# Kernel optimization log

Hardware: AMD Instinct MI355X
Metric: run time of the kernel (lower is better)

Reference implementation:

```python
import jax, jax.numpy as jnp
import numpy as np

N_NODES = 32768
N_EDGES = 524288
IN_CH = 128
OUT_CH = 128
EDGE_CH = 64
HIDDEN = 128


def setup_inputs() -> dict:
    key = jax.random.key(0)
    ks = jax.random.split(key, 8)
    x = jax.random.normal(ks[0], (N_NODES, IN_CH), dtype=jnp.float32)
    edge_index = jax.random.randint(ks[1], (2, N_EDGES), 0, N_NODES, dtype=jnp.int64)
    edge_attr = jax.random.uniform(ks[2], (N_EDGES, EDGE_CH), dtype=jnp.float32)
    # filter_network: Linear(edge_ch, hidden) -> tanh -> Linear(hidden, out)
    s1 = 1.0 / np.sqrt(EDGE_CH)
    s2 = 1.0 / np.sqrt(HIDDEN)
    W1 = jax.random.uniform(ks[3], (EDGE_CH, HIDDEN), jnp.float32, -s1, s1)
    b1 = jax.random.uniform(ks[4], (HIDDEN,), jnp.float32, -s1, s1)
    W2 = jax.random.uniform(ks[5], (HIDDEN, OUT_CH), jnp.float32, -s2, s2)
    b2 = jax.random.uniform(ks[6], (OUT_CH,), jnp.float32, -s2, s2)
    # attention_vector [out, 1], xavier_uniform with gain 1.414
    lim = 1.414 * np.sqrt(6.0 / (OUT_CH + 1))
    attn = jax.random.uniform(ks[7], (OUT_CH,), jnp.float32, -lim, lim)
    return {"x": x, "edge_index": edge_index, "edge_attr": edge_attr,
            "W1": W1, "b1": b1, "W2": W2, "b2": b2, "attn": attn}


def _segment_softmax(scores, segment_ids, num_segments):
    # PyG-style numerically stable softmax over segments
    seg_max = jax.ops.segment_max(scores, segment_ids, num_segments=num_segments)
    seg_max = jnp.where(jnp.isfinite(seg_max), seg_max, 0.0)
    e = jnp.exp(scores - seg_max[segment_ids])
    denom = jax.ops.segment_sum(e, segment_ids, num_segments=num_segments)
    return e / (denom[segment_ids] + 1e-16)


def reference(x, edge_index, edge_attr, W1, b1, W2, b2, attn):
    source, target = edge_index[0], edge_index[1]
    n_nodes = x.shape[0]
    source_features = x[source]                                  # [E, in]
    edge_attr_norm = edge_attr / (jnp.linalg.norm(edge_attr, axis=-1, keepdims=True) + 1e-8)
    h = jnp.tanh(edge_attr_norm @ W1 + b1)                       # [E, hidden]
    edge_filters = h @ W2 + b2                                   # [E, out]
    messages = source_features * edge_filters                    # [E, out]
    attention_scores = messages @ attn                           # [E]
    attention_weights = _segment_softmax(attention_scores, target, n_nodes)
    messages = messages * attention_weights[:, None]
    output = jax.ops.segment_sum(messages, target, num_segments=n_nodes)  # [N, out]
    return output, attention_weights
```

## Files before the change

kernel.cpp:

```cpp
#include <hip/hip_runtime.h>
#include <stdint.h>

typedef short short8 __attribute__((ext_vector_type(8)));
typedef float f32x16 __attribute__((ext_vector_type(16)));
typedef unsigned ux4 __attribute__((ext_vector_type(4)));

__device__ __forceinline__ unsigned cvtpk(float lo, float hi){
  unsigned r;
  asm("v_cvt_pk_bf16_f32 %0, %1, %2" : "=v"(r) : "v"(lo), "v"(hi));
  return r;
}

__device__ __forceinline__ short8 frag_from(unsigned a, unsigned b, unsigned c, unsigned d){
  union { unsigned u[4]; short8 s; } t;
  t.u[0] = a; t.u[1] = b; t.u[2] = c; t.u[3] = d;
  return t.s;
}

__global__ void k_setup(const float* __restrict__ x, uint2* __restrict__ xb, int n4,
                        const int* __restrict__ ei, int* __restrict__ rowptr, int E,
                        const float* __restrict__ W1, const float* __restrict__ W2,
                        ux4* __restrict__ Wf)
{
  const long long tid = (long long)blockIdx.x * 256 + threadIdx.x;
  if (tid < 48 * 64) {
    const int f = (int)(tid >> 6), l = (int)(tid & 63);
    const int r = l & 31, hh = l >> 5;
    float v[8];
    if (f < 16) {
      const int mf = f >> 2, ks = f & 3;
      const int c = 32 * mf + r, kb = ks * 16 + hh * 8;
#pragma unroll
      for (int j = 0; j < 8; ++j) v[j] = W1[(kb + j) * 128 + c];
    } else {
      const int f2 = f - 16, mf2 = f2 >> 3, ks = f2 & 7;
      const int o = 32 * mf2 + r, cb = ks * 16 + hh * 8;
#pragma unroll
      for (int j = 0; j < 8; ++j) v[j] = W2[(cb + j) * 128 + o];
    }
    ux4 d;
    d.x = cvtpk(v[0], v[1]); d.y = cvtpk(v[2], v[3]);
    d.z = cvtpk(v[4], v[5]); d.w = cvtpk(v[6], v[7]);
    Wf[(long long)f * 64 + l] = d;
  }
  const long long tot = (n4 > E) ? n4 : E;
  for (long long i = tid; i < tot; i += (long long)gridDim.x * 256) {
    if (i < n4) {
      float4 v = ((const float4*)x)[i];
      uint2 o; o.x = cvtpk(v.x, v.y); o.y = cvtpk(v.z, v.w);
      xb[i] = o;
    }
    if (i < E) atomicAdd(&rowptr[ei[E + i]], 1);
  }
}

__global__ __launch_bounds__(1024)
void k_scan(int* __restrict__ p, int N){
  __shared__ int ls[1024];
  const int t = threadIdx.x;
  const int chunk = (N + 1023) >> 10;
  const int c0 = t * chunk, c1 = min(N, c0 + chunk);
  int s = 0;
  for (int i = c0; i < c1; ++i) s += p[i];
  ls[t] = s;
  __syncthreads();
  for (int off = 1; off < 1024; off <<= 1) {
    int add = (t >= off) ? ls[t - off] : 0;
    __syncthreads();
    ls[t] += add;
    __syncthreads();
  }
  int run = (t == 0) ? 0 : ls[t - 1];
  for (int i = c0; i < c1; ++i) { int v = p[i]; p[i] = run; run += v; }
}

__global__ void k_fill(const int* __restrict__ ei, int* __restrict__ rowptr,
                       int* __restrict__ pose, int* __restrict__ eidx, int E){
  for (long long i = (long long)blockIdx.x * 256 + threadIdx.x; i < E;
       i += (long long)gridDim.x * 256) {
    int tg = ei[E + i];
    int pos = atomicAdd(&rowptr[tg], 1);
    if (pose) pose[i] = pos;
    eidx[pos] = (int)i;
  }
}

#define K1B 512
__global__ __launch_bounds__(K1B)
void k1_fused(const unsigned* __restrict__ xb, const int* __restrict__ ei,
              const float* __restrict__ ea, const ux4* __restrict__ Wf,
              const float* __restrict__ b1, const float* __restrict__ b2,
              const float* __restrict__ attn, const int* __restrict__ eidx,
              unsigned* __restrict__ msgp, float* __restrict__ scoreS, int E)
{
  __shared__ ux4 sWf[48 * 64];
  for (int i = threadIdx.x; i < 48 * 64; i += K1B) sWf[i] = Wf[i];
  __syncthreads();

  const int lane = threadIdx.x & 63;
  const int wv   = threadIdx.x >> 6;
  const int h    = lane >> 5;
  const int r31  = lane & 31;
  const long long gstep = (long long)gridDim.x * (K1B / 64) * 32;
  long long p = ((long long)blockIdx.x * (K1B / 64) + wv) * 32 + r31;
  if (p - r31 >= E) return;

  int eC = eidx[(p < E) ? p : (long long)(E - 1)];
  int srcC = ei[eC];
  unsigned ebC[4][4]; float rinC;
  {
    const float* er = ea + (long long)eC * 64 + h * 8;
    float4 v[8];
#pragma unroll
    for (int ks = 0; ks < 4; ++ks) {
      v[2*ks]   = *(const float4*)(er + ks * 16);
      v[2*ks+1] = *(const float4*)(er + ks * 16 + 4);
    }
    float ss = 0.f;
#pragma unroll
    for (int k8 = 0; k8 < 8; ++k8) {
      ss = fmaf(v[k8].x, v[k8].x, ss); ss = fmaf(v[k8].y, v[k8].y, ss);
      ss = fmaf(v[k8].z, v[k8].z, ss); ss = fmaf(v[k8].w, v[k8].w, ss);
    }
    ss += __shfl_xor(ss, 32);
    rinC = 1.0f / (sqrtf(ss) + 1e-8f);
#pragma unroll
    for (int ks = 0; ks < 4; ++ks) {
      ebC[ks][0] = cvtpk(v[2*ks].x,   v[2*ks].y);
      ebC[ks][1] = cvtpk(v[2*ks].z,   v[2*ks].w);
      ebC[ks][2] = cvtpk(v[2*ks+1].x, v[2*ks+1].y);
      ebC[ks][3] = cvtpk(v[2*ks+1].z, v[2*ks+1].w);
    }
  }
  long long pn = p + gstep;
  bool hasN = (pn - r31) < E;
  int eN = 0;
  if (hasN) eN = eidx[(pn < E) ? pn : (long long)(E - 1)];

  while (true) {
    float4 eaN[8]; int srcN = 0;
    if (hasN) {
      srcN = ei[eN];
      const float* er = ea + (long long)eN * 64 + h * 8;
#pragma unroll
      for (int ks = 0; ks < 4; ++ks) {
        eaN[2*ks]   = *(const float4*)(er + ks * 16);
        eaN[2*ks+1] = *(const float4*)(er + ks * 16 + 4);
      }
    }
    long long pnn = pn + gstep;
    bool hasNN = hasN && ((pnn - r31) < E);
    int eNN = 0;
    if (hasNN) eNN = eidx[(pnn < E) ? pnn : (long long)(E - 1)];

    const unsigned* xrow = xb + (long long)srcC * 64;
    uint2 xw[4];
#pragma unroll
    for (int rq = 0; rq < 4; ++rq)
      xw[rq] = *(const uint2*)(xrow + (8*rq + 4*h) / 2);
    asm volatile("" ::: "memory");

    unsigned hb[8][4];
#pragma unroll
    for (int mf = 0; mf < 4; ++mf) {
      f32x16 a1;
#pragma unroll
      for (int i = 0; i < 16; ++i) a1[i] = 0.f;
#pragma unroll
      for (int ks = 0; ks < 4; ++ks) {
        ux4 w = sWf[(mf * 4 + ks) * 64 + lane];
        a1 = __builtin_amdgcn_mfma_f32_32x32x16_bf16(
            frag_from(w.x, w.y, w.z, w.w),
            frag_from(ebC[ks][0], ebC[ks][1], ebC[ks][2], ebC[ks][3]), a1, 0, 0, 0);
      }
      float hv[16];
#pragma unroll
      for (int rq = 0; rq < 4; ++rq) {
        float4 bc = *(const float4*)(b1 + 32*mf + 8*rq + 4*h);
#pragma unroll
        for (int i = 0; i < 4; ++i) {
          float pre = fmaf(a1[rq*4+i], rinC, ((const float*)&bc)[i]);
          float e2  = __expf(2.0f * pre);
          hv[rq*4+i] = 1.0f - 2.0f / (e2 + 1.0f);
        }
      }
#pragma unroll
      for (int q = 0; q < 2; ++q) {
        unsigned A = cvtpk(hv[q*8+0], hv[q*8+1]);
        unsigned B = cvtpk(hv[q*8+2], hv[q*8+3]);
        unsigned C = cvtpk(hv[q*8+4], hv[q*8+5]);
        unsigned D = cvtpk(hv[q*8+6], hv[q*8+7]);
        unsigned Axr = (unsigned)__shfl_xor((int)A, 32);
        unsigned Bxr = (unsigned)__shfl_xor((int)B, 32);
        unsigned Cxr = (unsigned)__shfl_xor((int)C, 32);
        unsigned Dxr = (unsigned)__shfl_xor((int)D, 32);
        hb[2*mf+q][0] = h ? Cxr : A;
        hb[2*mf+q][1] = h ? Dxr : B;
        hb[2*mf+q][2] = h ? C   : Axr;
        hb[2*mf+q][3] = h ? D   : Bxr;
      }
    }

    float score = 0.f;
#pragma unroll
    for (int mf2 = 0; mf2 < 4; ++mf2) {
      uint2 xwN[4];
      if (mf2 < 3) {
#pragma unroll
        for (int rq = 0; rq < 4; ++rq)
          xwN[rq] = *(const uint2*)(xrow + (32*(mf2+1) + 8*rq + 4*h) / 2);
      }
      f32x16 a2;
#pragma unroll
      for (int i = 0; i < 16; ++i) a2[i] = 0.f;
#pragma unroll
      for (int ks = 0; ks < 8; ++ks) {
        ux4 w = sWf[(16 + mf2 * 8 + ks) * 64 + lane];
        a2 = __builtin_amdgcn_mfma_f32_32x32x16_bf16(
            frag_from(w.x, w.y, w.z, w.w),
            frag_from(hb[ks][0], hb[ks][1], hb[ks][2], hb[ks][3]), a2, 0, 0, 0);
      }
      unsigned pk[8];
#pragma unroll
      for (int rq = 0; rq < 4; ++rq) {
        const int o0 = 32*mf2 + 8*rq + 4*h;
        float4 b2c = *(const float4*)(b2 + o0);
        float4 atc = *(const float4*)(attn + o0);
        float x0 = __uint_as_float(xw[rq].x << 16);
        float x1 = __uint_as_float(xw[rq].x & 0xffff0000u);
        float x2 = __uint_as_float(xw[rq].y << 16);
        float x3 = __uint_as_float(xw[rq].y & 0xffff0000u);
        float m0 = (a2[rq*4+0] + b2c.x) * x0;
        float m1 = (a2[rq*4+1] + b2c.y) * x1;
        float m2 = (a2[rq*4+2] + b2c.z) * x2;
        float m3 = (a2[rq*4+3] + b2c.w) * x3;
        score = fmaf(m0, atc.x, score);
        score = fmaf(m1, atc.y, score);
        score = fmaf(m2, atc.z, score);
        score = fmaf(m3, atc.w, score);
        pk[2*rq]   = cvtpk(m0, m1);
        pk[2*rq+1] = cvtpk(m2, m3);
      }
      if (p < E) {
        ux4* dst = (ux4*)(msgp + p * 64 + 16*mf2 + 8*h);
        ux4 s0, s1;
        s0.x = pk[0]; s0.y = pk[1]; s0.z = pk[2]; s0.w = pk[3];
        s1.x = pk[4]; s1.y = pk[5]; s1.z = pk[6]; s1.w = pk[7];
        dst[0] = s0; dst[1] = s1;
      }
      if (mf2 < 3) {
#pragma unroll
        for (int rq = 0; rq < 4; ++rq) xw[rq] = xwN[rq];
      }
    }
    score += __shfl_xor(score, 32);
    if (h == 0 && p < E) scoreS[p] = score;

    if (!hasN) break;
    float ss = 0.f;
#pragma unroll
    for (int k8 = 0; k8 < 8; ++k8) {
      ss = fmaf(eaN[k8].x, eaN[k8].x, ss); ss = fmaf(eaN[k8].y, eaN[k8].y, ss);
      ss = fmaf(eaN[k8].z, eaN[k8].z, ss); ss = fmaf(eaN[k8].w, eaN[k8].w, ss);
    }
    ss += __shfl_xor(ss, 32);
    rinC = 1.0f / (sqrtf(ss) + 1e-8f);
#pragma unroll
    for (int ks = 0; ks < 4; ++ks) {
      ebC[ks][0] = cvtpk(eaN[2*ks].x,   eaN[2*ks].y);
      ebC[ks][1] = cvtpk(eaN[2*ks].z,   eaN[2*ks].w);
      ebC[ks][2] = cvtpk(eaN[2*ks+1].x, eaN[2*ks+1].y);
      ebC[ks][3] = cvtpk(eaN[2*ks+1].z, eaN[2*ks+1].w);
    }
    srcC = srcN; p = pn; pn = pnn; hasN = hasNN; eN = eNN;
  }
}

template<int FUSEW>
__global__ __launch_bounds__(256)
void k_gather(const unsigned* __restrict__ msgp, const float* __restrict__ scoreS,
              const int* __restrict__ rowptr, const int* __restrict__ eidx,
              float* __restrict__ lse, float* __restrict__ wreg,
              float* __restrict__ out, int N)
{
  const int lane = threadIdx.x & 63;
  const int node = blockIdx.x * 4 + (threadIdx.x >> 6);
  if (node >= N) return;
  const int end   = rowptr[node];
  const int start = node ? rowptr[node - 1] : 0;
  const int L     = end - start;

  float2 acc; acc.x = 0.f; acc.y = 0.f;

  if (L <= 64) {
    float sc = (lane < L) ? scoreS[start + lane] : -3.4e38f;
    float mn = sc;
#pragma unroll
    for (int off = 32; off; off >>= 1) mn = fmaxf(mn, __shfl_xor(mn, off));
    float ex = (lane < L) ? __expf(sc - mn) : 0.f;
    float s = ex;
#pragma unroll
    for (int off = 32; off; off >>= 1) s += __shfl_xor(s, off);
    const float w = ex / (s + 1e-16f);
    if (FUSEW) {
      if (lane < L) wreg[eidx[start + lane]] = w;
    } else if (lane == 0) {
      lse[node] = mn + logf(s + 1e-16f);
    }
#pragma unroll 4
    for (int j2 = 0; j2 < L; ++j2) {
      float wj = __shfl(w, j2);
      unsigned md = msgp[(long long)(start + j2) * 64 + lane];
      acc.x = fmaf(wj, __uint_as_float(md << 16),          acc.x);
      acc.y = fmaf(wj, __uint_as_float(md & 0xffff0000u), acc.y);
    }
  } else {
    float m = -3.4e38f, s = 0.f;
    for (int c0 = 0; c0 < L; c0 += 64) {
      const int j = c0 + lane;
      float sc = (j < L) ? scoreS[start + j] : -3.4e38f;
      float cm = sc;
#pragma unroll
      for (int off = 32; off; off >>= 1) cm = fmaxf(cm, __shfl_xor(cm, off));
      const float mn = fmaxf(m, cm);
      float ex = (j < L) ? __expf(sc - mn) : 0.f;
#pragma unroll
      for (int off = 32; off; off >>= 1) ex += __shfl_xor(ex, off);
      s = s * __expf(m - mn) + ex;
      m = mn;
    }
    const float lsev = m + logf(s + 1e-16f);
    if (!FUSEW && lane == 0) lse[node] = lsev;

    for (int c0 = 0; c0 < L; c0 += 64) {
      const int j = c0 + lane;
      float w = (j < L) ? __expf(scoreS[start + j] - lsev) : 0.f;
      if (FUSEW && j < L) wreg[eidx[start + j]] = w;
      const int jn = min(64, L - c0);
#pragma unroll 4
      for (int j2 = 0; j2 < jn; ++j2) {
        float wj = __shfl(w, j2);
        unsigned md = msgp[(long long)(start + c0 + j2) * 64 + lane];
        acc.x = fmaf(wj, __uint_as_float(md << 16),          acc.x);
        acc.y = fmaf(wj, __uint_as_float(md & 0xffff0000u), acc.y);
      }
    }
  }
  const int mf2 = lane >> 4, hh = (lane >> 3) & 1, rq = (lane >> 1) & 3, half = lane & 1;
  const int ch0 = 32*mf2 + 8*rq + 4*hh + 2*half;
  *(float2*)(out + (long long)node * 128 + ch0) = acc;
}

__global__ void k_wfin(int* __restrict__ pw, const int* __restrict__ ei,
                       const float* __restrict__ scoreS, const float* __restrict__ lse,
                       int E){
  for (long long i = (long long)blockIdx.x * 256 + threadIdx.x; i < E;
       i += (long long)gridDim.x * 256) {
    int pos = pw[i];
    float w = __expf(scoreS[pos] - lse[ei[E + i]]);
    pw[i] = __float_as_int(w);
  }
}

extern "C" void kernel_launch(void* const* d_in, const int* in_sizes, int n_in,
                              void* d_out, int out_size, void* d_ws, size_t ws_size,
                              hipStream_t stream)
{
  const float* x    = (const float*)d_in[0];
  const int*   ei   = (const int*)d_in[1];
  const float* ea   = (const float*)d_in[2];
  const float* W1   = (const float*)d_in[3];
  const float* b1   = (const float*)d_in[4];
  const float* W2   = (const float*)d_in[5];
  const float* b2   = (const float*)d_in[6];
  const float* attn = (const float*)d_in[7];
  const int N = in_sizes[0] / 128;
  const int E = in_sizes[2] / 64;
  if (E <= 0 || N <= 0) return;

  float* out   = (float*)d_out;
  float* wregN = out + (long long)N * 128;
  ux4*     Wf     = (ux4*)d_out;
  size_t   offE   = 65536;
  int*     eidxDO = (int*)((char*)d_out + offE);
  size_t   offX   = (offE + (size_t)E * 4 + 255) & ~(size_t)255;
  unsigned* xb    = (unsigned*)((char*)d_out + offX);

  char* wsb = (char*)d_ws;
  unsigned* msgp   = (unsigned*)wsb;
  float*    scoreS = (float*)(wsb + (size_t)E * 256);
  int*      rowptr = (int*)(wsb + (size_t)E * 260);
  float*    lse    = (float*)(wsb + (size_t)E * 260 + (size_t)N * 4);
  int*      eidxWS = (int*)(wsb + (size_t)E * 260 + (size_t)N * 8);
  const size_t need1 = (size_t)E * 260 + (size_t)N * 8;
  const size_t need2 = need1 + (size_t)E * 4;
  if (ws_size < need1) return;
  if ((size_t)out_size < (size_t)N * 128 + (size_t)E) return;
  if ((size_t)N * 512 < offX + (size_t)N * 256) return;

  const bool fused = (ws_size >= need2);
  int* eidx = fused ? eidxWS : eidxDO;

  (void)hipMemsetAsync(rowptr, 0, (size_t)N * 4, stream);
  k_setup<<<1024, 256, 0, stream>>>(x, (uint2*)xb, N * 32, ei, rowptr, E, W1, W2, Wf);
  k_scan<<<1, 1024, 0, stream>>>(rowptr, N);
  k_fill<<<1024, 256, 0, stream>>>(ei, rowptr, fused ? nullptr : (int*)wregN, eidx, E);
  const long long nwaves = ((long long)E + 31) / 32;
  const int grid = (int)min((long long)512, (nwaves + (K1B/64) - 1) / (K1B/64));
  k1_fused<<<grid, K1B, 0, stream>>>(xb, ei, ea, Wf, b1, b2, attn,
                                     eidx, msgp, scoreS, E);
  if (fused) {
    k_gather<1><<<(N + 3) / 4, 256, 0, stream>>>(msgp, scoreS, rowptr, eidx,
                                                 lse, wregN, out, N);
  } else {
    k_gather<0><<<(N + 3) / 4, 256, 0, stream>>>(msgp, scoreS, rowptr, eidx,
                                                 lse, wregN, out, N);
    k_wfin<<<1024, 256, 0, stream>>>((int*)wregN, ei, scoreS, lse, E);
  }
}
```

Baseline: 267.6 us.

## Fuse edge MLP and per-node softmax aggregation into one tiled LDS kernel

Replaces the separate edge-MLP kernel and gather kernel with one kernel. Each block takes windows of CSR-sorted edges (about WIN edges snapped to node boundaries), computes messages into LDS in a swizzled layout, then does the segment softmax and weighted sum directly from LDS. This removes the global round trip of the bf16 message buffer (E×256 bytes) and one launch. Nodes with more than CAP edges fall back to a chunked online-softmax path across the whole block. In exchange it loses the software prefetch pipelining of the old MLP loop, uses 1024-thread blocks with large LDS and a grid of at most 256 blocks, and tile boundaries come from atomicMin in the scan.

```diff
diff --git a/kernel.cpp b/kernel.cpp
--- a/kernel.cpp
+++ b/kernel.cpp
@@ -4,6 +4,19 @@
 typedef short short8 __attribute__((ext_vector_type(8)));
 typedef float f32x16 __attribute__((ext_vector_type(16)));
 typedef unsigned ux4 __attribute__((ext_vector_type(4)));
+
+#define WIN  288
+#define CAP  384
+#define FBLK 1024
+
+#define OFF_WF    0
+#define OFF_MSG   49152
+#define OFF_SC    (OFF_MSG + CAP*64*4)
+#define OFF_RED   (OFF_SC + CAP*4)
+#define OFF_CTL   (OFF_RED + 64)
+#define OFF_PART  (OFF_CTL + 16)
+#define OFF_ACC   (OFF_PART + 16*128*4)
+#define LDS_TOT   (OFF_ACC + 512)
 
 __device__ __forceinline__ unsigned cvtpk(float lo, float hi){
   unsigned r;
@@ -55,7 +68,7 @@
 }
 
 __global__ __launch_bounds__(1024)
-void k_scan(int* __restrict__ p, int N){
+void k_scan(int* __restrict__ p, int N, int* __restrict__ tileFirst, int ntiles){
   __shared__ int ls[1024];
   const int t = threadIdx.x;
   const int chunk = (N + 1023) >> 10;
@@ -71,294 +84,339 @@
     __syncthreads();
   }
   int run = (t == 0) ? 0 : ls[t - 1];
-  for (int i = c0; i < c1; ++i) { int v = p[i]; p[i] = run; run += v; }
+  for (int i = c0; i < c1; ++i) {
+    int v = p[i];
+    p[i] = run;
+    int tw = run / WIN;
+    if (tw > ntiles - 1) tw = ntiles - 1;
+    atomicMin(&tileFirst[tw], i);
+    run += v;
+  }
 }
 
 __global__ void k_fill(const int* __restrict__ ei, int* __restrict__ rowptr,
-                       int* __restrict__ pose, int* __restrict__ eidx, int E){
+                       int* __restrict__ eidx, int E){
   for (long long i = (long long)blockIdx.x * 256 + threadIdx.x; i < E;
        i += (long long)gridDim.x * 256) {
     int tg = ei[E + i];
     int pos = atomicAdd(&rowptr[tg], 1);
-    if (pose) pose[i] = pos;
     eidx[pos] = (int)i;
   }
 }
 
-#define K1B 512
-__global__ __launch_bounds__(K1B)
-void k1_fused(const unsigned* __restrict__ xb, const int* __restrict__ ei,
-              const float* __restrict__ ea, const ux4* __restrict__ Wf,
-              const float* __restrict__ b1, const float* __restrict__ b2,
-              const float* __restrict__ attn, const int* __restrict__ eidx,
-              unsigned* __restrict__ msgp, float* __restrict__ scoreS, int E)
+__device__ __forceinline__ void mlp_chunk(
+    int e0, int cnt, int oversized,
+    const unsigned* __restrict__ xb, const int* __restrict__ ei,
+    const float* __restrict__ ea, const float* __restrict__ b1,
+    const float* __restrict__ b2, const float* __restrict__ attn,
+    const int* __restrict__ eidx, float* __restrict__ scoreS,
+    const ux4* sWf, unsigned* sMsg, float* sScore,
+    int lane, int wv, int h, int r31)
 {
-  __shared__ ux4 sWf[48 * 64];
-  for (int i = threadIdx.x; i < 48 * 64; i += K1B) sWf[i] = Wf[i];
-  __syncthreads();
-
-  const int lane = threadIdx.x & 63;
-  const int wv   = threadIdx.x >> 6;
+  if (wv * 32 >= cnt) return;
+  const int li  = wv * 32 + r31;
+  const int lic = (li < cnt) ? li : (cnt - 1);
+  const long long p = (long long)e0 + lic;
+  const int e   = eidx[p];
+  const int src = ei[e];
+
+  const float* er = ea + (long long)e * 64 + h * 8;
+  float4 v[8];
+#pragma unroll
+  for (int ks = 0; ks < 4; ++ks) {
+    v[2*ks]   = *(const float4*)(er + ks * 16);
+    v[2*ks+1] = *(const float4*)(er + ks * 16 + 4);
+  }
+  float ss = 0.f;
+#pragma unroll
+  for (int k8 = 0; k8 < 8; ++k8) {
+    ss = fmaf(v[k8].x, v[k8].x, ss); ss = fmaf(v[k8].y, v[k8].y, ss);
+    ss = fmaf(v[k8].z, v[k8].z, ss); ss = fmaf(v[k8].w, v[k8].w, ss);
+  }
+  ss += __shfl_xor(ss, 32);
+  const float rin = 1.0f / (sqrtf(ss) + 1e-8f);
+  unsigned eb[4][4];
+#pragma unroll
+  for (int ks = 0; ks < 4; ++ks) {
+    eb[ks][0] = cvtpk(v[2*ks].x,   v[2*ks].y);
+    eb[ks][1] = cvtpk(v[2*ks].z,   v[2*ks].w);
+    eb[ks][2] = cvtpk(v[2*ks+1].x, v[2*ks+1].y);
+    eb[ks][3] = cvtpk(v[2*ks+1].z, v[2*ks+1].w);
+  }
+
+  unsigned hb[8][4];
+#pragma unroll
+  for (int mf = 0; mf < 4; ++mf) {
+    f32x16 a1;
+#pragma unroll
+    for (int i = 0; i < 16; ++i) a1[i] = 0.f;
+#pragma unroll
+    for (int ks = 0; ks < 4; ++ks) {
+      ux4 w = sWf[(mf * 4 + ks) * 64 + lane];
+      a1 = __builtin_amdgcn_mfma_f32_32x32x16_bf16(
+          frag_from(w.x, w.y, w.z, w.w),
+          frag_from(eb[ks][0], eb[ks][1], eb[ks][2], eb[ks][3]), a1, 0, 0, 0);
+    }
+    float hv[16];
+#pragma unroll
+    for (int rq = 0; rq < 4; ++rq) {
+      float4 bc = *(const float4*)(b1 + 32*mf + 8*rq + 4*h);
+#pragma unroll
+      for (int i = 0; i < 4; ++i) {
+        float pre = fmaf(a1[rq*4+i], rin, ((const float*)&bc)[i]);
+        float e2  = __expf(2.0f * pre);
+        hv[rq*4+i] = 1.0f - 2.0f / (e2 + 1.0f);
+      }
+    }
+#pragma unroll
+    for (int q = 0; q < 2; ++q) {
+      unsigned A = cvtpk(hv[q*8+0], hv[q*8+1]);
+      unsigned B = cvtpk(hv[q*8+2], hv[q*8+3]);
+      unsigned C = cvtpk(hv[q*8+4], hv[q*8+5]);
+      unsigned D = cvtpk(hv[q*8+6], hv[q*8+7]);
+      unsigned Axr = (unsigned)__shfl_xor((int)A, 32);
+      unsigned Bxr = (unsigned)__shfl_xor((int)B, 32);
+      unsigned Cxr = (unsigned)__shfl_xor((int)C, 32);
+      unsigned Dxr = (unsigned)__shfl_xor((int)D, 32);
+      hb[2*mf+q][0] = h ? Cxr : A;
+      hb[2*mf+q][1] = h ? Dxr : B;
+      hb[2*mf+q][2] = h ? C   : Axr;
+      hb[2*mf+q][3] = h ? D   : Bxr;
+    }
+  }
+
+  const unsigned* xrow = xb + (long long)src * 64;
+  float score = 0.f;
+#pragma unroll
+  for (int mf2 = 0; mf2 < 4; ++mf2) {
+    uint2 xw[4];
+#pragma unroll
+    for (int rq = 0; rq < 4; ++rq)
+      xw[rq] = *(const uint2*)(xrow + (32*mf2 + 8*rq + 4*h) / 2);
+    f32x16 a2;
+#pragma unroll
+    for (int i = 0; i < 16; ++i) a2[i] = 0.f;
+#pragma unroll
+    for (int ks = 0; ks < 8; ++ks) {
+      ux4 w = sWf[(16 + mf2 * 8 + ks) * 64 + lane];
+      a2 = __builtin_amdgcn_mfma_f32_32x32x16_bf16(
+          frag_from(w.x, w.y, w.z, w.w),
+          frag_from(hb[ks][0], hb[ks][1], hb[ks][2], hb[ks][3]), a2, 0, 0, 0);
+    }
+    unsigned pk[8];
+#pragma unroll
+    for (int rq = 0; rq < 4; ++rq) {
+      const int o0 = 32*mf2 + 8*rq + 4*h;
+      float4 b2c = *(const float4*)(b2 + o0);
+      float4 atc = *(const float4*)(attn + o0);
+      float x0 = __uint_as_float(xw[rq].x << 16);
+      float x1 = __uint_as_float(xw[rq].x & 0xffff0000u);
+      float x2 = __uint_as_float(xw[rq].y << 16);
+      float x3 = __uint_as_float(xw[rq].y & 0xffff0000u);
+      float m0 = (a2[rq*4+0] + b2c.x) * x0;
+      float m1 = (a2[rq*4+1] + b2c.y) * x1;
+      float m2 = (a2[rq*4+2] + b2c.z) * x2;
+      float m3 = (a2[rq*4+3] + b2c.w) * x3;
+      score = fmaf(m0, atc.x, score);
+      score = fmaf(m1, atc.y, score);
+      score = fmaf(m2, atc.z, score);
+      score = fmaf(m3, atc.w, score);
+      pk[2*rq]   = cvtpk(m0, m1);
+      pk[2*rq+1] = cvtpk(m2, m3);
+    }
+    const int s0slot = 4*mf2 + 2*h;
+    const int m15 = li & 15;
+    ux4 q0, q1;
+    q0.x = pk[0]; q0.y = pk[1]; q0.z = pk[2]; q0.w = pk[3];
+    q1.x = pk[4]; q1.y = pk[5]; q1.z = pk[6]; q1.w = pk[7];
+    *(ux4*)&sMsg[li*64 + ((s0slot     ^ m15) << 2)] = q0;
+    *(ux4*)&sMsg[li*64 + (((s0slot+1) ^ m15) << 2)] = q1;
+  }
+  score += __shfl_xor(score, 32);
+  if (h == 0) {
+    sScore[li] = score;
+    if (oversized && li < cnt) scoreS[p] = score;
+  }
+}
+
+__device__ __forceinline__ unsigned msg_ld(const unsigned* sMsg, int row, int lane){
+  return sMsg[row*64 + ((((lane>>2) ^ (row & 15)) << 2) | (lane & 3))];
+}
+
+__global__ __launch_bounds__(FBLK)
+void k_fused(const unsigned* __restrict__ xb, const int* __restrict__ ei,
+             const float* __restrict__ ea, const ux4* __restrict__ Wf,
+             const float* __restrict__ b1, const float* __restrict__ b2,
+             const float* __restrict__ attn, const int* __restrict__ eidx,
+             const int* __restrict__ rowptr, const int* __restrict__ tileFirst,
+             float* __restrict__ scoreS, float* __restrict__ wreg,
+             float* __restrict__ out, int N, int E, int ntiles)
+{
+  extern __shared__ char smem[];
+  ux4*      sWf    = (ux4*)(smem + OFF_WF);
+  unsigned* sMsg   = (unsigned*)(smem + OFF_MSG);
+  float*    sScore = (float*)(smem + OFF_SC);
+  float*    sRed   = (float*)(smem + OFF_RED);
+  float*    sCtl   = (float*)(smem + OFF_CTL);
+  float*    sPart  = (float*)(smem + OFF_PART);
+  float*    sAcc   = (float*)(smem + OFF_ACC);
+
+  const int tid  = threadIdx.x;
+  const int lane = tid & 63;
+  const int wv   = tid >> 6;
   const int h    = lane >> 5;
   const int r31  = lane & 31;
-  const long long gstep = (long long)gridDim.x * (K1B / 64) * 32;
-  long long p = ((long long)blockIdx.x * (K1B / 64) + wv) * 32 + r31;
-  if (p - r31 >= E) return;
-
-  int eC = eidx[(p < E) ? p : (long long)(E - 1)];
-  int srcC = ei[eC];
-  unsigned ebC[4][4]; float rinC;
-  {
-    const float* er = ea + (long long)eC * 64 + h * 8;
-    float4 v[8];
-#pragma unroll
-    for (int ks = 0; ks < 4; ++ks) {
-      v[2*ks]   = *(const float4*)(er + ks * 16);
-      v[2*ks+1] = *(const float4*)(er + ks * 16 + 4);
-    }
-    float ss = 0.f;
-#pragma unroll
-    for (int k8 = 0; k8 < 8; ++k8) {
-      ss = fmaf(v[k8].x, v[k8].x, ss); ss = fmaf(v[k8].y, v[k8].y, ss);
-      ss = fmaf(v[k8].z, v[k8].z, ss); ss = fmaf(v[k8].w, v[k8].w, ss);
-    }
-    ss += __shfl_xor(ss, 32);
-    rinC = 1.0f / (sqrtf(ss) + 1e-8f);
-#pragma unroll
-    for (int ks = 0; ks < 4; ++ks) {
-      ebC[ks][0] = cvtpk(v[2*ks].x,   v[2*ks].y);
-      ebC[ks][1] = cvtpk(v[2*ks].z,   v[2*ks].w);
-      ebC[ks][2] = cvtpk(v[2*ks+1].x, v[2*ks+1].y);
-      ebC[ks][3] = cvtpk(v[2*ks+1].z, v[2*ks+1].w);
-    }
-  }
-  long long pn = p + gstep;
-  bool hasN = (pn - r31) < E;
-  int eN = 0;
-  if (hasN) eN = eidx[(pn < E) ? pn : (long long)(E - 1)];
-
-  while (true) {
-    float4 eaN[8]; int srcN = 0;
-    if (hasN) {
-      srcN = ei[eN];
-      const float* er = ea + (long long)eN * 64 + h * 8;
-#pragma unroll
-      for (int ks = 0; ks < 4; ++ks) {
-        eaN[2*ks]   = *(const float4*)(er + ks * 16);
-        eaN[2*ks+1] = *(const float4*)(er + ks * 16 + 4);
+
+  for (int i = tid; i < 48*64; i += FBLK) sWf[i] = Wf[i];
+  __syncthreads();
+
+  for (int t = blockIdx.x; t < ntiles; t += gridDim.x) {
+    const int nF = tileFirst[t];
+    if (nF >= N) continue;
+    int t2 = t + 1;
+    while (t2 < ntiles && tileFirst[t2] >= N) ++t2;
+    const int nL = (t2 < ntiles) ? tileFirst[t2] - 1 : N - 1;
+
+    int n  = nF;
+    int s0 = n ? rowptr[n-1] : 0;
+    while (n <= nL) {
+      const int en = rowptr[n];
+      const int dn = en - s0;
+      if (dn > CAP) {
+        if (tid < 128) sAcc[tid] = 0.f;
+        if (tid == 0) { sCtl[0] = -3.4e38f; sCtl[1] = 0.f; }
+        __syncthreads();
+        for (int c0 = 0; c0 < dn; c0 += CAP) {
+          const int cnt = min(CAP, dn - c0);
+          mlp_chunk(s0 + c0, cnt, 1, xb, ei, ea, b1, b2, attn, eidx, scoreS,
+                    sWf, sMsg, sScore, lane, wv, h, r31);
+          __syncthreads();
+          float vmax = (tid < cnt) ? sScore[tid] : -3.4e38f;
+#pragma unroll
+          for (int off = 32; off; off >>= 1) vmax = fmaxf(vmax, __shfl_xor(vmax, off));
+          if (lane == 0) sRed[wv] = vmax;
+          __syncthreads();
+          if (tid == 0) {
+            float cm = sRed[0];
+            for (int w = 1; w < 16; ++w) cm = fmaxf(cm, sRed[w]);
+            float mn = fmaxf(sCtl[0], cm);
+            sCtl[2] = __expf(sCtl[0] - mn);
+            sCtl[0] = mn;
+          }
+          __syncthreads();
+          const float mn = sCtl[0], r = sCtl[2];
+          float ev = (tid < cnt) ? __expf(sScore[tid] - mn) : 0.f;
+#pragma unroll
+          for (int off = 32; off; off >>= 1) ev += __shfl_xor(ev, off);
+          if (lane == 0) sRed[wv] = ev;
+          float2 pacc; pacc.x = 0.f; pacc.y = 0.f;
+          if (wv * 32 < cnt) {
+            float pl = (lane < 32 && wv*32 + lane < cnt)
+                     ? __expf(sScore[wv*32 + lane] - mn) : 0.f;
+            const int jn = min(32, cnt - wv*32);
+            for (int j2 = 0; j2 < jn; ++j2) {
+              float pj = __shfl(pl, j2);
+              unsigned md = msg_ld(sMsg, wv*32 + j2, lane);
+              pacc.x = fmaf(pj, __uint_as_float(md << 16),          pacc.x);
+              pacc.y = fmaf(pj, __uint_as_float(md & 0xffff0000u), pacc.y);
+            }
+          }
+          sPart[wv*128 + 2*lane]     = pacc.x;
+          sPart[wv*128 + 2*lane + 1] = pacc.y;
+          __syncthreads();
+          if (tid == 0) {
+            float ssum = 0.f;
+            for (int w = 0; w < 16; ++w) ssum += sRed[w];
+            sCtl[1] = sCtl[1] * sCtl[2] + ssum;
+          }
+          if (tid < 128) {
+            float tp = 0.f;
+            for (int w = 0; w < 16; ++w) tp += sPart[w*128 + tid];
+            sAcc[tid] = sAcc[tid] * r + tp;
+          }
+          __syncthreads();
+        }
+        const float mfin = sCtl[0];
+        const float sfin = sCtl[1] + 1e-16f;
+        for (int j = tid; j < dn; j += FBLK)
+          wreg[eidx[s0 + j]] = __expf(scoreS[s0 + j] - mfin) / sfin;
+        if (tid < 64) {
+          const int mf2 = tid >> 4, hh = (tid >> 3) & 1, rq = (tid >> 1) & 3, hf = tid & 1;
+          const int ch0 = 32*mf2 + 8*rq + 4*hh + 2*hf;
+          float2 o; o.x = sAcc[2*tid]; o.y = sAcc[2*tid + 1];
+          *(float2*)(out + (long long)n * 128 + ch0) = o;
+        }
+        __syncthreads();
+        s0 = en; ++n;
+        continue;
       }
-    }
-    long long pnn = pn + gstep;
-    bool hasNN = hasN && ((pnn - r31) < E);
-    int eNN = 0;
-    if (hasNN) eNN = eidx[(pnn < E) ? pnn : (long long)(E - 1)];
-
-    const unsigned* xrow = xb + (long long)srcC * 64;
-    uint2 xw[4];
-#pragma unroll
-    for (int rq = 0; rq < 4; ++rq)
-      xw[rq] = *(const uint2*)(xrow + (8*rq + 4*h) / 2);
-    asm volatile("" ::: "memory");
-
-    unsigned hb[8][4];
-#pragma unroll
-    for (int mf = 0; mf < 4; ++mf) {
-      f32x16 a1;
-#pragma unroll
-      for (int i = 0; i < 16; ++i) a1[i] = 0.f;
-#pragma unroll
-      for (int ks = 0; ks < 4; ++ks) {
-        ux4 w = sWf[(mf * 4 + ks) * 64 + lane];
-        a1 = __builtin_amdgcn_mfma_f32_32x32x16_bf16(
-            frag_from(w.x, w.y, w.z, w.w),
-            frag_from(ebC[ks][0], ebC[ks][1], ebC[ks][2], ebC[ks][3]), a1, 0, 0, 0);
+      int m = n, send = en;
+      while (m < nL) {
+        int nx = rowptr[m + 1];
+        if (nx - s0 > CAP) break;
+        send = nx; ++m;
       }
-      float hv[16];
-#pragma unroll
-      for (int rq = 0; rq < 4; ++rq) {
-        float4 bc = *(const float4*)(b1 + 32*mf + 8*rq + 4*h);
-#pragma unroll
-        for (int i = 0; i < 4; ++i) {
-          float pre = fmaf(a1[rq*4+i], rinC, ((const float*)&bc)[i]);
-          float e2  = __expf(2.0f * pre);
-          hv[rq*4+i] = 1.0f - 2.0f / (e2 + 1.0f);
+      mlp_chunk(s0, send - s0, 0, xb, ei, ea, b1, b2, attn, eidx, scoreS,
+                sWf, sMsg, sScore, lane, wv, h, r31);
+      __syncthreads();
+      for (int nn = n + wv; nn <= m; nn += 16) {
+        const int gs = nn ? rowptr[nn - 1] : 0;
+        const int L  = rowptr[nn] - gs;
+        const int ls = gs - s0;
+        float2 acc; acc.x = 0.f; acc.y = 0.f;
+        if (L <= 64) {
+          float sc = (lane < L) ? sScore[ls + lane] : -3.4e38f;
+          float mn = sc;
+#pragma unroll
+          for (int off = 32; off; off >>= 1) mn = fmaxf(mn, __shfl_xor(mn, off));
+          float ex = (lane < L) ? __expf(sc - mn) : 0.f;
+          float s = ex;
+#pragma unroll
+          for (int off = 32; off; off >>= 1) s += __shfl_xor(s, off);
+          const float w = ex / (s + 1e-16f);
+          if (lane < L) wreg[eidx[gs + lane]] = w;
+          for (int j2 = 0; j2 < L; ++j2) {
+            float wj = __shfl(w, j2);
+            unsigned md = msg_ld(sMsg, ls + j2, lane);
+            acc.x = fmaf(wj, __uint_as_float(md << 16),          acc.x);
+            acc.y = fmaf(wj, __uint_as_float(md & 0xffff0000u), acc.y);
+          }
+        } else {
+          float mr = -3.4e38f, s = 0.f;
+          for (int c0 = 0; c0 < L; c0 += 64) {
+            const int j = c0 + lane;
+            float sc = (j < L) ? sScore[ls + j] : -3.4e38f;
+            float cm = sc;
+#pragma unroll
+            for (int off = 32; off; off >>= 1) cm = fmaxf(cm, __shfl_xor(cm, off));
+            const float mn = fmaxf(mr, cm);
+            float ex = (j < L) ? __expf(sc - mn) : 0.f;
+#pragma unroll
+            for (int off = 32; off; off >>= 1) ex += __shfl_xor(ex, off);
+            s = s * __expf(mr - mn) + ex;
+            mr = mn;
+          }
+          const float inv = 1.0f / (s + 1e-16f);
+          for (int c0 = 0; c0 < L; c0 += 64) {
+            const int j = c0 + lane;
+            float w = (j < L) ? __expf(sScore[ls + j] - mr) * inv : 0.f;
+            if (j < L) wreg[eidx[gs + j]] = w;
+            const int jn = min(64, L - c0);
+            for (int j2 = 0; j2 < jn; ++j2) {
+              float wj = __shfl(w, j2);
+              unsigned md = msg_ld(sMsg, ls + c0 + j2, lane);
+              acc.x = fmaf(wj, __uint_as_float(md << 16),          acc.x);
+              acc.y = fmaf(wj, __uint_as_float(md & 0xffff0000u), acc.y);
+            }
+          }
         }
+        const int mf2 = lane >> 4, hh = (lane >> 3) & 1, rq = (lane >> 1) & 3, hf = lane & 1;
+        const int ch0 = 32*mf2 + 8*rq + 4*hh + 2*hf;
+        *(float2*)(out + (long long)nn * 128 + ch0) = acc;
       }
-#pragma unroll
-      for (int q = 0; q < 2; ++q) {
-        unsigned A = cvtpk(hv[q*8+0], hv[q*8+1]);
-        unsigned B = cvtpk(hv[q*8+2], hv[q*8+3]);
-        unsigned C = cvtpk(hv[q*8+4], hv[q*8+5]);
-        unsigned D = cvtpk(hv[q*8+6], hv[q*8+7]);
-        unsigned Axr = (unsigned)__shfl_xor((int)A, 32);
-        unsigned Bxr = (unsigned)__shfl_xor((int)B, 32);
-        unsigned Cxr = (unsigned)__shfl_xor((int)C, 32);
-        unsigned Dxr = (unsigned)__shfl_xor((int)D, 32);
-        hb[2*mf+q][0] = h ? Cxr : A;
-        hb[2*mf+q][1] = h ? Dxr : B;
-        hb[2*mf+q][2] = h ? C   : Axr;
-        hb[2*mf+q][3] = h ? D   : Bxr;
-      }
-    }
-
-    float score = 0.f;
-#pragma unroll
-    for (int mf2 = 0; mf2 < 4; ++mf2) {
-      uint2 xwN[4];
-      if (mf2 < 3) {
-#pragma unroll
-        for (int rq = 0; rq < 4; ++rq)
-          xwN[rq] = *(const uint2*)(xrow + (32*(mf2+1) + 8*rq + 4*h) / 2);
-      }
-      f32x16 a2;
-#pragma unroll
-      for (int i = 0; i < 16; ++i) a2[i] = 0.f;
-#pragma unroll
-      for (int ks = 0; ks < 8; ++ks) {
-        ux4 w = sWf[(16 + mf2 * 8 + ks) * 64 + lane];
-        a2 = __builtin_amdgcn_mfma_f32_32x32x16_bf16(
-            frag_from(w.x, w.y, w.z, w.w),
-            frag_from(hb[ks][0], hb[ks][1], hb[ks][2], hb[ks][3]), a2, 0, 0, 0);
-      }
-      unsigned pk[8];
-#pragma unroll
-      for (int rq = 0; rq < 4; ++rq) {
-        const int o0 = 32*mf2 + 8*rq + 4*h;
-        float4 b2c = *(const float4*)(b2 + o0);
-        float4 atc = *(const float4*)(attn + o0);
-        float x0 = __uint_as_float(xw[rq].x << 16);
-        float x1 = __uint_as_float(xw[rq].x & 0xffff0000u);
-        float x2 = __uint_as_float(xw[rq].y << 16);
-        float x3 = __uint_as_float(xw[rq].y & 0xffff0000u);
-        float m0 = (a2[rq*4+0] + b2c.x) * x0;
-        float m1 = (a2[rq*4+1] + b2c.y) * x1;
-        float m2 = (a2[rq*4+2] + b2c.z) * x2;
-        float m3 = (a2[rq*4+3] + b2c.w) * x3;
-        score = fmaf(m0, atc.x, score);
-        score = fmaf(m1, atc.y, score);
-        score = fmaf(m2, atc.z, score);
-        score = fmaf(m3, atc.w, score);
-        pk[2*rq]   = cvtpk(m0, m1);
-        pk[2*rq+1] = cvtpk(m2, m3);
-      }
-      if (p < E) {
-        ux4* dst = (ux4*)(msgp + p * 64 + 16*mf2 + 8*h);
-        ux4 s0, s1;
-        s0.x = pk[0]; s0.y = pk[1]; s0.z = pk[2]; s0.w = pk[3];
-        s1.x = pk[4]; s1.y = pk[5]; s1.z = pk[6]; s1.w = pk[7];
-        dst[0] = s0; dst[1] = s1;
-      }
-      if (mf2 < 3) {
-#pragma unroll
-        for (int rq = 0; rq < 4; ++rq) xw[rq] = xwN[rq];
-      }
-    }
-    score += __shfl_xor(score, 32);
-    if (h == 0 && p < E) scoreS[p] = score;
-
-    if (!hasN) break;
-    float ss = 0.f;
-#pragma unroll
-    for (int k8 = 0; k8 < 8; ++k8) {
-      ss = fmaf(eaN[k8].x, eaN[k8].x, ss); ss = fmaf(eaN[k8].y, eaN[k8].y, ss);
-      ss = fmaf(eaN[k8].z, eaN[k8].z, ss); ss = fmaf(eaN[k8].w, eaN[k8].w, ss);
-    }
-    ss += __shfl_xor(ss, 32);
-    rinC = 1.0f / (sqrtf(ss) + 1e-8f);
-#pragma unroll
-    for (int ks = 0; ks < 4; ++ks) {
-      ebC[ks][0] = cvtpk(eaN[2*ks].x,   eaN[2*ks].y);
-      ebC[ks][1] = cvtpk(eaN[2*ks].z,   eaN[2*ks].w);
-      ebC[ks][2] = cvtpk(eaN[2*ks+1].x, eaN[2*ks+1].y);
-      ebC[ks][3] = cvtpk(eaN[2*ks+1].z, eaN[2*ks+1].w);
-    }
-    srcC = srcN; p = pn; pn = pnn; hasN = hasNN; eN = eNN;
-  }
-}
-
-template<int FUSEW>
-__global__ __launch_bounds__(256)
-void k_gather(const unsigned* __restrict__ msgp, const float* __restrict__ scoreS,
-              const int* __restrict__ rowptr, const int* __restrict__ eidx,
-              float* __restrict__ lse, float* __restrict__ wreg,
-              float* __restrict__ out, int N)
-{
-  const int lane = threadIdx.x & 63;
-  const int node = blockIdx.x * 4 + (threadIdx.x >> 6);
-  if (node >= N) return;
-  const int end   = rowptr[node];
-  const int start = node ? rowptr[node - 1] : 0;
-  const int L     = end - start;
-
-  float2 acc; acc.x = 0.f; acc.y = 0.f;
-
-  if (L <= 64) {
-    float sc = (lane < L) ? scoreS[start + lane] : -3.4e38f;
-    float mn = sc;
-#pragma unroll
-    for (int off = 32; off; off >>= 1) mn = fmaxf(mn, __shfl_xor(mn, off));
-    float ex = (lane < L) ? __expf(sc - mn) : 0.f;
-    float s = ex;
-#pragma unroll
-    for (int off = 32; off; off >>= 1) s += __shfl_xor(s, off);
-    const float w = ex / (s + 1e-16f);
-    if (FUSEW) {
-      if (lane < L) wreg[eidx[start + lane]] = w;
-    } else if (lane == 0) {
-      lse[node] = mn + logf(s + 1e-16f);
-    }
-#pragma unroll 4
-    for (int j2 = 0; j2 < L; ++j2) {
-      float wj = __shfl(w, j2);
-      unsigned md = msgp[(long long)(start + j2) * 64 + lane];
-      acc.x = fmaf(wj, __uint_as_float(md << 16),          acc.x);
-      acc.y = fmaf(wj, __uint_as_float(md & 0xffff0000u), acc.y);
-    }
-  } else {
-    float m = -3.4e38f, s = 0.f;
-    for (int c0 = 0; c0 < L; c0 += 64) {
-      const int j = c0 + lane;
-      float sc = (j < L) ? scoreS[start + j] : -3.4e38f;
-      float cm = sc;
-#pragma unroll
-      for (int off = 32; off; off >>= 1) cm = fmaxf(cm, __shfl_xor(cm, off));
-      const float mn = fmaxf(m, cm);
-      float ex = (j < L) ? __expf(sc - mn) : 0.f;
-#pragma unroll
-      for (int off = 32; off; off >>= 1) ex += __shfl_xor(ex, off);
-      s = s * __expf(m - mn) + ex;
-      m = mn;
-    }
-    const float lsev = m + logf(s + 1e-16f);
-    if (!FUSEW && lane == 0) lse[node] = lsev;
-
-    for (int c0 = 0; c0 < L; c0 += 64) {
-      const int j = c0 + lane;
-      float w = (j < L) ? __expf(scoreS[start + j] - lsev) : 0.f;
-      if (FUSEW && j < L) wreg[eidx[start + j]] = w;
-      const int jn = min(64, L - c0);
-#pragma unroll 4
-      for (int j2 = 0; j2 < jn; ++j2) {
-        float wj = __shfl(w, j2);
-        unsigned md = msgp[(long long)(start + c0 + j2) * 64 + lane];
-        acc.x = fmaf(wj, __uint_as_float(md << 16),          acc.x);
-        acc.y = fmaf(wj, __uint_as_float(md & 0xffff0000u), acc.y);
-      }
-    }
-  }
-  const int mf2 = lane >> 4, hh = (lane >> 3) & 1, rq = (lane >> 1) & 3, half = lane & 1;
-  const int ch0 = 32*mf2 + 8*rq + 4*hh + 2*half;
-  *(float2*)(out + (long long)node * 128 + ch0) = acc;
-}
-
-__global__ void k_wfin(int* __restrict__ pw, const int* __restrict__ ei,
-                       const float* __restrict__ scoreS, const float* __restrict__ lse,
-                       int E){
-  for (long long i = (long long)blockIdx.x * 256 + threadIdx.x; i < E;
-       i += (long long)gridDim.x * 256) {
-    int pos = pw[i];
-    float w = __expf(scoreS[pos] - lse[ei[E + i]]);
-    pw[i] = __float_as_int(w);
+      __syncthreads();
+      s0 = send; n = m + 1;
+    }
   }
 }
 
@@ -377,44 +435,39 @@
   const int N = in_sizes[0] / 128;
   const int E = in_sizes[2] / 64;
   if (E <= 0 || N <= 0) return;
-
-  float* out   = (float*)d_out;
-  float* wregN = out + (long long)N * 128;
-  ux4*     Wf     = (ux4*)d_out;
-  size_t   offE   = 65536;
-  int*     eidxDO = (int*)((char*)d_out + offE);
-  size_t   offX   = (offE + (size_t)E * 4 + 255) & ~(size_t)255;
-  unsigned* xb    = (unsigned*)((char*)d_out + offX);
-
+  const int ntiles = (E + WIN - 1) / WIN;
+
+  float* out  = (float*)d_out;
+  float* wreg = out + (long long)N * 128;
+
+  auto al = [](size_t v){ return (v + 255) & ~(size_t)255; };
   char* wsb = (char*)d_ws;
-  unsigned* msgp   = (unsigned*)wsb;
-  float*    scoreS = (float*)(wsb + (size_t)E * 256);
-  int*      rowptr = (int*)(wsb + (size_t)E * 260);
-  float*    lse    = (float*)(wsb + (size_t)E * 260 + (size_t)N * 4);
-  int*      eidxWS = (int*)(wsb + (size_t)E * 260 + (size_t)N * 8);
-  const size_t need1 = (size_t)E * 260 + (size_t)N * 8;
-  const size_t need2 = need1 + (size_t)E * 4;
-  if (ws_size < need1) return;
+  size_t oRow  = 0;
+  size_t oTile = al(oRow + (size_t)N * 4);
+  size_t oEidx = al(oTile + (size_t)ntiles * 4);
+  size_t oScr  = al(oEidx + (size_t)E * 4);
+  size_t oXb   = al(oScr + (size_t)E * 4);
+  size_t oWf   = al(oXb + (size_t)N * 256);
+  size_t need  = oWf + 49152;
+  if (ws_size < need) return;
   if ((size_t)out_size < (size_t)N * 128 + (size_t)E) return;
-  if ((size_t)N * 512 < offX + (size_t)N * 256) return;
-
-  const bool fused = (ws_size >= need2);
-  int* eidx = fused ? eidxWS : eidxDO;
+
+  int*      rowptr    = (int*)(wsb + oRow);
+  int*      tileFirst = (int*)(wsb + oTile);
+  int*      eidx      = (int*)(wsb + oEidx);
+  float*    scoreS    = (float*)(wsb + oScr);
+  unsigned* xb        = (unsigned*)(wsb + oXb);
+  ux4*      Wf        = (ux4*)(wsb + oWf);
 
   (void)hipMemsetAsync(rowptr, 0, (size_t)N * 4, stream);
+  (void)hipMemsetAsync(tileFirst, 0x7F, (size_t)ntiles * 4, stream);
   k_setup<<<1024, 256, 0, stream>>>(x, (uint2*)xb, N * 32, ei, rowptr, E, W1, W2, Wf);
-  k_scan<<<1, 1024, 0, stream>>>(rowptr, N);
-  k_fill<<<1024, 256, 0, stream>>>(ei, rowptr, fused ? nullptr : (int*)wregN, eidx, E);
-  const long long nwaves = ((long long)E + 31) / 32;
-  const int grid = (int)min((long long)512, (nwaves + (K1B/64) - 1) / (K1B/64));
-  k1_fused<<<grid, K1B, 0, stream>>>(xb, ei, ea, Wf, b1, b2, attn,
-                                     eidx, msgp, scoreS, E);
-  if (fused) {
-    k_gather<1><<<(N + 3) / 4, 256, 0, stream>>>(msgp, scoreS, rowptr, eidx,
-                                                 lse, wregN, out, N);
-  } else {
-    k_gather<0><<<(N + 3) / 4, 256, 0, stream>>>(msgp, scoreS, rowptr, eidx,
-                                                 lse, wregN, out, N);
-    k_wfin<<<1024, 256, 0, stream>>>((int*)wregN, ei, scoreS, lse, E);
-  }
-}
+  k_scan<<<1, 1024, 0, stream>>>(rowptr, N, tileFirst, ntiles);
+  k_fill<<<1024, 256, 0, stream>>>(ei, rowptr, eidx, E);
+  (void)hipFuncSetAttribute(reinterpret_cast<const void*>(&k_fused),
+                            hipFuncAttributeMaxDynamicSharedMemorySize, LDS_TOT);
+  const int grid = min(256, ntiles);
+  k_fused<<<grid, FBLK, LDS_TOT, stream>>>(xb, ei, ea, Wf, b1, b2, attn,
+                                           eidx, rowptr, tileFirst,
+                                           scoreS, wreg, out, N, E, ntiles);
+}
```

New measurement: 327.9 us. 1.23x slower.

## Process edges in source-sorted order and scatter messages to target-sorted slots

Applied to the files above, without the earlier changes.

Adds a second CSR built over source nodes, so the fused message kernel walks edges grouped by source. Consecutive edges then reuse the same x rows, which should improve gather locality. Each message and score is written to the edge's target-sorted slot through a stored position array, so the gather kernel still reads contiguously. It also drops the non-fused fallback path and the separate weight-finalize kernel. The cost is extra atomics, a second scan, and scattered writes of messages and scores.

```diff
diff --git a/kernel.cpp b/kernel.cpp
--- a/kernel.cpp
+++ b/kernel.cpp
@@ -18,7 +18,8 @@
 }
 
 __global__ void k_setup(const float* __restrict__ x, uint2* __restrict__ xb, int n4,
-                        const int* __restrict__ ei, int* __restrict__ rowptr, int E,
+                        const int* __restrict__ ei, int* __restrict__ rowptr,
+                        int* __restrict__ srcptr, int E,
                         const float* __restrict__ W1, const float* __restrict__ W2,
                         ux4* __restrict__ Wf)
 {
@@ -50,38 +51,50 @@
       uint2 o; o.x = cvtpk(v.x, v.y); o.y = cvtpk(v.z, v.w);
       xb[i] = o;
     }
-    if (i < E) atomicAdd(&rowptr[ei[E + i]], 1);
+    if (i < E) {
+      atomicAdd(&rowptr[ei[E + i]], 1);
+      atomicAdd(&srcptr[ei[i]], 1);
+    }
   }
 }
 
 __global__ __launch_bounds__(1024)
-void k_scan(int* __restrict__ p, int N){
+void k_scan2(int* __restrict__ p1, int* __restrict__ p2, int N){
   __shared__ int ls[1024];
   const int t = threadIdx.x;
   const int chunk = (N + 1023) >> 10;
   const int c0 = t * chunk, c1 = min(N, c0 + chunk);
-  int s = 0;
-  for (int i = c0; i < c1; ++i) s += p[i];
-  ls[t] = s;
-  __syncthreads();
-  for (int off = 1; off < 1024; off <<= 1) {
-    int add = (t >= off) ? ls[t - off] : 0;
+#pragma unroll 1
+  for (int a = 0; a < 2; ++a) {
+    int* p = a ? p2 : p1;
+    int s = 0;
+    for (int i = c0; i < c1; ++i) s += p[i];
+    ls[t] = s;
     __syncthreads();
-    ls[t] += add;
+    for (int off = 1; off < 1024; off <<= 1) {
+      int add = (t >= off) ? ls[t - off] : 0;
+      __syncthreads();
+      ls[t] += add;
+      __syncthreads();
+    }
+    int run = (t == 0) ? 0 : ls[t - 1];
+    for (int i = c0; i < c1; ++i) { int v = p[i]; p[i] = run; run += v; }
     __syncthreads();
   }
-  int run = (t == 0) ? 0 : ls[t - 1];
-  for (int i = c0; i < c1; ++i) { int v = p[i]; p[i] = run; run += v; }
 }
 
 __global__ void k_fill(const int* __restrict__ ei, int* __restrict__ rowptr,
-                       int* __restrict__ pose, int* __restrict__ eidx, int E){
+                       int* __restrict__ srcptr, int* __restrict__ eidx,
+                       int* __restrict__ pose, int* __restrict__ esrc, int E){
   for (long long i = (long long)blockIdx.x * 256 + threadIdx.x; i < E;
        i += (long long)gridDim.x * 256) {
     int tg = ei[E + i];
     int pos = atomicAdd(&rowptr[tg], 1);
-    if (pose) pose[i] = pos;
+    pose[i] = pos;
     eidx[pos] = (int)i;
+    int sc = ei[i];
+    int sp = atomicAdd(&srcptr[sc], 1);
+    esrc[sp] = (int)i;
   }
 }
 
@@ -90,7 +103,8 @@
 void k1_fused(const unsigned* __restrict__ xb, const int* __restrict__ ei,
               const float* __restrict__ ea, const ux4* __restrict__ Wf,
               const float* __restrict__ b1, const float* __restrict__ b2,
-              const float* __restrict__ attn, const int* __restrict__ eidx,
+              const float* __restrict__ attn, const int* __restrict__ esrc,
+              const int* __restrict__ pose,
               unsigned* __restrict__ msgp, float* __restrict__ scoreS, int E)
 {
   __shared__ ux4 sWf[48 * 64];
@@ -105,8 +119,9 @@
   long long p = ((long long)blockIdx.x * (K1B / 64) + wv) * 32 + r31;
   if (p - r31 >= E) return;
 
-  int eC = eidx[(p < E) ? p : (long long)(E - 1)];
+  int eC = esrc[(p < E) ? p : (long long)(E - 1)];
   int srcC = ei[eC];
+  int posC = pose[eC];
   unsigned ebC[4][4]; float rinC;
   {
     const float* er = ea + (long long)eC * 64 + h * 8;
@@ -135,12 +150,13 @@
   long long pn = p + gstep;
   bool hasN = (pn - r31) < E;
   int eN = 0;
-  if (hasN) eN = eidx[(pn < E) ? pn : (long long)(E - 1)];
+  if (hasN) eN = esrc[(pn < E) ? pn : (long long)(E - 1)];
 
   while (true) {
-    float4 eaN[8]; int srcN = 0;
+    float4 eaN[8]; int srcN = 0, posN = 0;
     if (hasN) {
       srcN = ei[eN];
+      posN = pose[eN];
       const float* er = ea + (long long)eN * 64 + h * 8;
 #pragma unroll
       for (int ks = 0; ks < 4; ++ks) {
@@ -151,7 +167,7 @@
     long long pnn = pn + gstep;
     bool hasNN = hasN && ((pnn - r31) < E);
     int eNN = 0;
-    if (hasNN) eNN = eidx[(pnn < E) ? pnn : (long long)(E - 1)];
+    if (hasNN) eNN = esrc[(pnn < E) ? pnn : (long long)(E - 1)];
 
     const unsigned* xrow = xb + (long long)srcC * 64;
     uint2 xw[4];
@@ -242,7 +258,7 @@
         pk[2*rq+1] = cvtpk(m2, m3);
       }
       if (p < E) {
-        ux4* dst = (ux4*)(msgp + p * 64 + 16*mf2 + 8*h);
+        ux4* dst = (ux4*)(msgp + (long long)posC * 64 + 16*mf2 + 8*h);
         ux4 s0, s1;
         s0.x = pk[0]; s0.y = pk[1]; s0.z = pk[2]; s0.w = pk[3];
         s1.x = pk[4]; s1.y = pk[5]; s1.z = pk[6]; s1.w = pk[7];
@@ -254,7 +270,7 @@
       }
     }
     score += __shfl_xor(score, 32);
-    if (h == 0 && p < E) scoreS[p] = score;
+    if (h == 0 && p < E) scoreS[posC] = score;
 
     if (!hasN) break;
     float ss = 0.f;
@@ -272,16 +288,14 @@
       ebC[ks][2] = cvtpk(eaN[2*ks+1].x, eaN[2*ks+1].y);
       ebC[ks][3] = cvtpk(eaN[2*ks+1].z, eaN[2*ks+1].w);
     }
-    srcC = srcN; p = pn; pn = pnn; hasN = hasNN; eN = eNN;
-  }
-}
-
-template<int FUSEW>
+    srcC = srcN; posC = posN; p = pn; pn = pnn; hasN = hasNN; eN = eNN;
+  }
+}
+
 __global__ __launch_bounds__(256)
 void k_gather(const unsigned* __restrict__ msgp, const float* __restrict__ scoreS,
               const int* __restrict__ rowptr, const int* __restrict__ eidx,
-              float* __restrict__ lse, float* __restrict__ wreg,
-              float* __restrict__ out, int N)
+              float* __restrict__ wreg, float* __restrict__ out, int N)
 {
   const int lane = threadIdx.x & 63;
   const int node = blockIdx.x * 4 + (threadIdx.x >> 6);
@@ -302,11 +316,7 @@
 #pragma unroll
     for (int off = 32; off; off >>= 1) s += __shfl_xor(s, off);
     const float w = ex / (s + 1e-16f);
-    if (FUSEW) {
-      if (lane < L) wreg[eidx[start + lane]] = w;
-    } else if (lane == 0) {
-      lse[node] = mn + logf(s + 1e-16f);
-    }
+    if (lane < L) wreg[eidx[start + lane]] = w;
 #pragma unroll 4
     for (int j2 = 0; j2 < L; ++j2) {
       float wj = __shfl(w, j2);
@@ -329,13 +339,11 @@
       s = s * __expf(m - mn) + ex;
       m = mn;
     }
-    const float lsev = m + logf(s + 1e-16f);
-    if (!FUSEW && lane == 0) lse[node] = lsev;
-
+    const float inv = 1.0f / (s + 1e-16f);
     for (int c0 = 0; c0 < L; c0 += 64) {
       const int j = c0 + lane;
-      float w = (j < L) ? __expf(scoreS[start + j] - lsev) : 0.f;
-      if (FUSEW && j < L) wreg[eidx[start + j]] = w;
+      float w = (j < L) ? __expf(scoreS[start + j] - m) * inv : 0.f;
+      if (j < L) wreg[eidx[start + j]] = w;
       const int jn = min(64, L - c0);
 #pragma unroll 4
       for (int j2 = 0; j2 < jn; ++j2) {
@@ -349,17 +357,6 @@
   const int mf2 = lane >> 4, hh = (lane >> 3) & 1, rq = (lane >> 1) & 3, half = lane & 1;
   const int ch0 = 32*mf2 + 8*rq + 4*hh + 2*half;
   *(float2*)(out + (long long)node * 128 + ch0) = acc;
-}
-
-__global__ void k_wfin(int* __restrict__ pw, const int* __restrict__ ei,
-                       const float* __restrict__ scoreS, const float* __restrict__ lse,
-                       int E){
-  for (long long i = (long long)blockIdx.x * 256 + threadIdx.x; i < E;
-       i += (long long)gridDim.x * 256) {
-    int pos = pw[i];
-    float w = __expf(scoreS[pos] - lse[ei[E + i]]);
-    pw[i] = __float_as_int(w);
-  }
 }
 
 extern "C" void kernel_launch(void* const* d_in, const int* in_sizes, int n_in,
@@ -378,43 +375,36 @@
   const int E = in_sizes[2] / 64;
   if (E <= 0 || N <= 0) return;
 
-  float* out   = (float*)d_out;
-  float* wregN = out + (long long)N * 128;
-  ux4*     Wf     = (ux4*)d_out;
-  size_t   offE   = 65536;
-  int*     eidxDO = (int*)((char*)d_out + offE);
-  size_t   offX   = (offE + (size_t)E * 4 + 255) & ~(size_t)255;
-  unsigned* xb    = (unsigned*)((char*)d_out + offX);
+  float* out  = (float*)d_out;
+  float* wreg = out + (long long)N * 128;
+
+  ux4*      Wf   = (ux4*)d_out;
+  unsigned* xb   = (unsigned*)((char*)d_out + 65536);
+  size_t    offS = 65536 + (size_t)N * 256;
+  int*      esrc = (int*)((char*)d_out + offS);
+  int*      pose = (int*)((char*)d_out + offS + (size_t)E * 4);
+  const size_t doNeed = offS + (size_t)E * 8;
 
   char* wsb = (char*)d_ws;
   unsigned* msgp   = (unsigned*)wsb;
   float*    scoreS = (float*)(wsb + (size_t)E * 256);
   int*      rowptr = (int*)(wsb + (size_t)E * 260);
-  float*    lse    = (float*)(wsb + (size_t)E * 260 + (size_t)N * 4);
-  int*      eidxWS = (int*)(wsb + (size_t)E * 260 + (size_t)N * 8);
-  const size_t need1 = (size_t)E * 260 + (size_t)N * 8;
-  const size_t need2 = need1 + (size_t)E * 4;
-  if (ws_size < need1) return;
+  int*      srcptr = (int*)(wsb + (size_t)E * 260 + (size_t)N * 4);
+  int*      eidx   = (int*)(wsb + (size_t)E * 260 + (size_t)N * 8);
+  const size_t need = (size_t)E * 264 + (size_t)N * 8;
+  if (ws_size < need) return;
   if ((size_t)out_size < (size_t)N * 128 + (size_t)E) return;
-  if ((size_t)N * 512 < offX + (size_t)N * 256) return;
-
-  const bool fused = (ws_size >= need2);
-  int* eidx = fused ? eidxWS : eidxDO;
-
-  (void)hipMemsetAsync(rowptr, 0, (size_t)N * 4, stream);
-  k_setup<<<1024, 256, 0, stream>>>(x, (uint2*)xb, N * 32, ei, rowptr, E, W1, W2, Wf);
-  k_scan<<<1, 1024, 0, stream>>>(rowptr, N);
-  k_fill<<<1024, 256, 0, stream>>>(ei, rowptr, fused ? nullptr : (int*)wregN, eidx, E);
+  if ((size_t)N * 512 < doNeed) return;
+
+  (void)hipMemsetAsync(rowptr, 0, (size_t)N * 8, stream);
+  k_setup<<<1024, 256, 0, stream>>>(x, (uint2*)xb, N * 32, ei, rowptr, srcptr, E,
+                                    W1, W2, Wf);
+  k_scan2<<<1, 1024, 0, stream>>>(rowptr, srcptr, N);
+  k_fill<<<1024, 256, 0, stream>>>(ei, rowptr, srcptr, eidx, pose, esrc, E);
   const long long nwaves = ((long long)E + 31) / 32;
   const int grid = (int)min((long long)512, (nwaves + (K1B/64) - 1) / (K1B/64));
   k1_fused<<<grid, K1B, 0, stream>>>(xb, ei, ea, Wf, b1, b2, attn,
-                                     eidx, msgp, scoreS, E);
-  if (fused) {
-    k_gather<1><<<(N + 3) / 4, 256, 0, stream>>>(msgp, scoreS, rowptr, eidx,
-                                                 lse, wregN, out, N);
-  } else {
-    k_gather<0><<<(N + 3) / 4, 256, 0, stream>>>(msgp, scoreS, rowptr, eidx,
-                                                 lse, wregN, out, N);
-    k_wfin<<<1024, 256, 0, stream>>>((int*)wregN, ei, scoreS, lse, E);
-  }
-}
+                                     esrc, pose, msgp, scoreS, E);
+  k_gather<<<(N + 3) / 4, 256, 0, stream>>>(msgp, scoreS, rowptr, eidx,
+                                            wreg, out, N);
+}
```

Result: slower. 378.6 us (+41.4%).
